# Kernel tuning notes

Hardware: AMD Instinct MI355X
Metric: run time of the kernel (lower is better)

The kernel has to match this reference:

```python
import jax, jax.numpy as jnp
import numpy as np

B, T, D, E, WR, H = 4, 2048, 1024, 4, 128, 4096  # batch, seq, d_model, mem_experts, read width, fuse hidden
EPS = 1e-5


def _ln(u, g, b):
    mu = jnp.mean(u, axis=-1, keepdims=True)
    var = jnp.mean(jnp.square(u - mu), axis=-1, keepdims=True)
    return (u - mu) * jax.lax.rsqrt(var + EPS) * g + b


def setup_inputs() -> dict:
    key = jax.random.key(0)
    ks = jax.random.split(key, 8)
    s1 = 1.0 / np.sqrt(D + WR)
    s2 = 1.0 / np.sqrt(H)
    sg = 1.0 / np.sqrt((1 + E) * D)
    return {
        "x": jax.random.normal(ks[0], (B, T, D), jnp.float32),
        "vt": jax.random.normal(ks[1], (B, T, D), jnp.float32),
        "dts": jax.random.normal(ks[2], (E, B, T, D), jnp.float32),
        "r_feat": jax.random.normal(ks[3], (B, T, WR), jnp.float32),
        "fuse_ln_g": jnp.ones((D + WR,), jnp.float32),
        "fuse_ln_b": jnp.zeros((D + WR,), jnp.float32),
        "fuse_w1": jax.random.normal(ks[4], (D + WR, H), jnp.float32) * s1,
        "fuse_b1": jnp.zeros((H,), jnp.float32),
        "fuse_w2": jax.random.normal(ks[5], (H, D), jnp.float32) * s2,
        "fuse_b2": jnp.zeros((D,), jnp.float32),
        "pg_ln_g": jnp.ones(((1 + E) * D,), jnp.float32),
        "pg_ln_b": jnp.zeros(((1 + E) * D,), jnp.float32),
        "gate_w": jax.random.normal(ks[6], ((1 + E) * D, 1 + E), jnp.float32) * sg,
        "gate_b": jnp.concatenate([jnp.zeros((1,)), jnp.full((E,), -1.0)]).astype(jnp.float32),
    }


def reference(x, vt, dts, r_feat, fuse_ln_g, fuse_ln_b, fuse_w1, fuse_b1,
              fuse_w2, fuse_b2, pg_ln_g, pg_ln_b, gate_w, gate_b):
    # fusion branch: vt = vt + MLP(LN(cat(x, read_feat)))
    fuse_in = jnp.concatenate([x, r_feat], axis=-1)            # [B,T,D+WR]
    h = jax.nn.gelu(_ln(fuse_in, fuse_ln_g, fuse_ln_b) @ fuse_w1 + fuse_b1)
    vt = vt + (h @ fuse_w2 + fuse_b2)

    # paths = [vanilla] + mem experts -> [P,B,T,D], P = 1+E
    paths = jnp.concatenate([vt[None], dts], axis=0)
    z = jnp.moveaxis(paths, 0, -2).reshape(x.shape[0], x.shape[1], -1)  # cat over last dim
    logits = _ln(z, pg_ln_g, pg_ln_b) @ gate_w + gate_b        # temp = 1.0
    pi = jax.nn.softmax(logits, axis=-1)                        # [B,T,P]

    out = jnp.einsum('btp,pbtd->btd', pi, paths)
    g_mem = jnp.sum(pi[..., 1:], axis=-1, keepdims=True)        # synthetic memory gate
    return out, g_mem
```

## Files before the change

kernel.cpp:

```cpp
#include <hip/hip_runtime.h>
#include <hip/hip_bf16.h>

#define Bc 4
#define Tc 2048
#define Dc 1024
#define Ec 4
#define WRc 128
#define Hc 4096
#define Mc (Bc*Tc)
#define K1c (Dc+WRc)
#define Pc (1+Ec)
#define ZDc (Pc*Dc)
#define EPSc 1e-5f

typedef __attribute__((ext_vector_type(8))) short short8;
typedef __attribute__((ext_vector_type(4))) float f32x4;

__device__ __forceinline__ float wave_red_sum(float v) {
    #pragma unroll
    for (int o = 32; o > 0; o >>= 1) v += __shfl_down(v, o);
    return v;
}

__device__ __forceinline__ float gelu_tanh(float x) {
    const float c = 0.7978845608028654f;
    float x3 = x * x * x;
    return 0.5f * x * (1.0f + tanhf(c * (x + 0.044715f * x3)));
}

__global__ __launch_bounds__(256) void transpose_cast_kernel(
    const float* __restrict__ src, __hip_bfloat16* __restrict__ dst, int R, int C) {
    __shared__ float tile[32][33];
    int c0 = blockIdx.x * 32, r0 = blockIdx.y * 32;
    int tx = threadIdx.x, ty = threadIdx.y;
    #pragma unroll
    for (int i = ty; i < 32; i += 8)
        tile[i][tx] = src[(size_t)(r0 + i) * C + c0 + tx];
    __syncthreads();
    #pragma unroll
    for (int i = ty; i < 32; i += 8)
        dst[(size_t)(c0 + i) * R + r0 + tx] = __float2bfloat16(tile[tx][i]);
}

__global__ __launch_bounds__(256) void fuse_ln_kernel(
    const float* __restrict__ x, const float* __restrict__ rf,
    const float* __restrict__ g, const float* __restrict__ b,
    __hip_bfloat16* __restrict__ aln) {
    int row = blockIdx.x;
    int tid = threadIdx.x, lane = tid & 63, wave = tid >> 6;
    const float* xr = x + (size_t)row * Dc;
    const float* rr = rf + (size_t)row * WRc;

    float v[5];
    float s = 0.f, s2 = 0.f;
    #pragma unroll
    for (int i = 0; i < 4; i++) {
        int idx = tid + i * 256;
        float u = xr[idx];
        v[i] = u; s += u; s2 += u * u;
    }
    {
        int idx = tid + 1024;
        float u = (idx < K1c) ? rr[idx - Dc] : 0.f;
        v[4] = u; s += u; s2 += u * u;
    }
    __shared__ float red[8];
    float sw = wave_red_sum(s), s2w = wave_red_sum(s2);
    if (lane == 0) { red[wave] = sw; red[4 + wave] = s2w; }
    __syncthreads();
    float stot  = red[0] + red[1] + red[2] + red[3];
    float s2tot = red[4] + red[5] + red[6] + red[7];
    const float inv = 1.0f / (float)K1c;
    float mu = stot * inv;
    float var = s2tot * inv - mu * mu;
    float rstd = rsqrtf(var + EPSc);

    __hip_bfloat16* orow = aln + (size_t)row * K1c;
    #pragma unroll
    for (int i = 0; i < 4; i++) {
        int idx = tid + i * 256;
        orow[idx] = __float2bfloat16((v[i] - mu) * rstd * g[idx] + b[idx]);
    }
    {
        int idx = tid + 1024;
        if (idx < K1c)
            orow[idx] = __float2bfloat16((v[4] - mu) * rstd * g[idx] + b[idx]);
    }
}

template <int EPI>
__global__ __launch_bounds__(256) void gemm128_kernel(
    const __hip_bfloat16* __restrict__ A, const __hip_bfloat16* __restrict__ Bt,
    int K, int N, const float* __restrict__ bias, const float* __restrict__ add,
    void* __restrict__ outp) {
    __shared__ __hip_bfloat16 As[128 * 64];
    __shared__ __hip_bfloat16 Bs[128 * 64];
    const int tid  = threadIdx.x;
    const int lane = tid & 63;
    const int wave = tid >> 6;
    const int wr = wave >> 1, wc = wave & 1;
    const int m0 = blockIdx.y * 128;
    const int n0 = blockIdx.x * 128;

    f32x4 acc[4][4] = {};

    for (int k0 = 0; k0 < K; k0 += 64) {
        __syncthreads();
        #pragma unroll
        for (int i = 0; i < 4; i++) {
            int f = i * 256 + tid;
            int r = f >> 3, c8 = (f & 7) << 3;
            __builtin_amdgcn_global_load_lds(
                (const __attribute__((address_space(1))) void*)(A + (size_t)(m0 + r) * K + k0 + c8),
                (__attribute__((address_space(3))) void*)(As + f * 8), 16, 0, 0);
        }
        #pragma unroll
        for (int i = 0; i < 4; i++) {
            int f = i * 256 + tid;
            int r = f >> 3, c8 = (f & 7) << 3;
            __builtin_amdgcn_global_load_lds(
                (const __attribute__((address_space(1))) void*)(Bt + (size_t)(n0 + r) * K + k0 + c8),
                (__attribute__((address_space(3))) void*)(Bs + f * 8), 16, 0, 0);
        }
        __syncthreads();

        #pragma unroll
        for (int kk = 0; kk < 2; kk++) {
            short8 af[4], bfr[4];
            #pragma unroll
            for (int m = 0; m < 4; m++)
                af[m] = *(const short8*)(As + (wr * 64 + m * 16 + (lane & 15)) * 64 + kk * 32 + (lane >> 4) * 8);
            #pragma unroll
            for (int n = 0; n < 4; n++)
                bfr[n] = *(const short8*)(Bs + (wc * 64 + n * 16 + (lane & 15)) * 64 + kk * 32 + (lane >> 4) * 8);
            #pragma unroll
            for (int m = 0; m < 4; m++)
                #pragma unroll
                for (int n = 0; n < 4; n++)
                    acc[m][n] = __builtin_amdgcn_mfma_f32_16x16x32_bf16(af[m], bfr[n], acc[m][n], 0, 0, 0);
        }
    }

    #pragma unroll
    for (int m = 0; m < 4; m++) {
        int grow_base = m0 + wr * 64 + m * 16 + (lane >> 4) * 4;
        #pragma unroll
        for (int n = 0; n < 4; n++) {
            int gcol = n0 + wc * 64 + n * 16 + (lane & 15);
            float bv = bias[gcol];
            #pragma unroll
            for (int i = 0; i < 4; i++) {
                int grow = grow_base + i;
                float vv = acc[m][n][i] + bv;
                if (EPI == 0) {
                    ((__hip_bfloat16*)outp)[(size_t)grow * N + gcol] = __float2bfloat16(gelu_tanh(vv));
                } else {
                    ((float*)outp)[(size_t)grow * N + gcol] = vv + add[(size_t)grow * N + gcol];
                }
            }
        }
    }
}

__global__ __launch_bounds__(256) void gate_kernel(
    const float* __restrict__ vtn, const float* __restrict__ dts,
    const float* __restrict__ g, const float* __restrict__ b,
    const float* __restrict__ gw, const float* __restrict__ gb,
    float* __restrict__ out, float* __restrict__ gmem) {
    int row = blockIdx.x;
    int tid = threadIdx.x, lane = tid & 63, wave = tid >> 6;
    __shared__ float z[ZDc];
    __shared__ float red[8];
    __shared__ float lsum[5];
    if (tid < 5) lsum[tid] = 0.f;

    float s = 0.f, s2 = 0.f;
    #pragma unroll
    for (int k = 0; k < ZDc / 256; k++) {
        int i = tid + k * 256;
        int p = i >> 10, d = i & 1023;
        float u = (p == 0) ? vtn[(size_t)row * Dc + d]
                           : dts[((size_t)(p - 1) * Mc + row) * Dc + d];
        z[i] = u; s += u; s2 += u * u;
    }
    float sw = wave_red_sum(s), s2w = wave_red_sum(s2);
    if (lane == 0) { red[wave] = sw; red[4 + wave] = s2w; }
    __syncthreads();
    float stot  = red[0] + red[1] + red[2] + red[3];
    float s2tot = red[4] + red[5] + red[6] + red[7];
    const float inv = 1.0f / (float)ZDc;
    float mu = stot * inv;
    float var = s2tot * inv - mu * mu;
    float rstd = rsqrtf(var + EPSc);

    float lacc[5] = {0.f, 0.f, 0.f, 0.f, 0.f};
    #pragma unroll
    for (int k = 0; k < ZDc / 256; k++) {
        int i = tid + k * 256;
        float zh = (z[i] - mu) * rstd * g[i] + b[i];
        #pragma unroll
        for (int j = 0; j < 5; j++) lacc[j] += zh * gw[i * 5 + j];
    }
    #pragma unroll
    for (int j = 0; j < 5; j++) {
        float v = wave_red_sum(lacc[j]);
        if (lane == 0) atomicAdd(&lsum[j], v);
    }
    __syncthreads();

    float lg[5];
    #pragma unroll
    for (int j = 0; j < 5; j++) lg[j] = lsum[j] + gb[j];
    float mx = lg[0];
    #pragma unroll
    for (int j = 1; j < 5; j++) mx = fmaxf(mx, lg[j]);
    float ex[5], den = 0.f;
    #pragma unroll
    for (int j = 0; j < 5; j++) { ex[j] = expf(lg[j] - mx); den += ex[j]; }
    float rden = 1.0f / den;
    float pi[5];
    #pragma unroll
    for (int j = 0; j < 5; j++) pi[j] = ex[j] * rden;

    #pragma unroll
    for (int k = 0; k < Dc / 256; k++) {
        int d = tid + k * 256;
        float o = 0.f;
        #pragma unroll
        for (int p = 0; p < 5; p++) o += pi[p] * z[p * Dc + d];
        out[(size_t)row * Dc + d] = o;
    }
    if (tid == 0) gmem[row] = pi[1] + pi[2] + pi[3] + pi[4];
}

extern "C" void kernel_launch(void* const* d_in, const int* in_sizes, int n_in,
                              void* d_out, int out_size, void* d_ws, size_t ws_size,
                              hipStream_t stream) {
    const float* x    = (const float*)d_in[0];
    const float* vt   = (const float*)d_in[1];
    const float* dts  = (const float*)d_in[2];
    const float* rf   = (const float*)d_in[3];
    const float* flg  = (const float*)d_in[4];
    const float* flb  = (const float*)d_in[5];
    const float* w1   = (const float*)d_in[6];
    const float* b1   = (const float*)d_in[7];
    const float* w2   = (const float*)d_in[8];
    const float* b2   = (const float*)d_in[9];
    const float* plg  = (const float*)d_in[10];
    const float* plb  = (const float*)d_in[11];
    const float* gw   = (const float*)d_in[12];
    const float* gb   = (const float*)d_in[13];

    char* ws = (char*)d_ws;
    size_t off = 0;
    __hip_bfloat16* w1t = (__hip_bfloat16*)(ws + off); off += (size_t)Hc * K1c * 2;
    __hip_bfloat16* w2t = (__hip_bfloat16*)(ws + off); off += (size_t)Dc * Hc * 2;
    __hip_bfloat16* aln = (__hip_bfloat16*)(ws + off); off += (size_t)Mc * K1c * 2;
    __hip_bfloat16* h   = (__hip_bfloat16*)(ws + off); off += (size_t)Mc * Hc * 2;
    float*          vtn = (float*)(ws + off);          off += (size_t)Mc * Dc * 4;

    transpose_cast_kernel<<<dim3(Hc / 32, K1c / 32), dim3(32, 8), 0, stream>>>(w1, w1t, K1c, Hc);
    transpose_cast_kernel<<<dim3(Dc / 32, Hc / 32), dim3(32, 8), 0, stream>>>(w2, w2t, Hc, Dc);

    fuse_ln_kernel<<<Mc, 256, 0, stream>>>(x, rf, flg, flb, aln);

    gemm128_kernel<0><<<dim3(Hc / 128, Mc / 128), 256, 0, stream>>>(aln, w1t, K1c, Hc, b1, nullptr, h);

    gemm128_kernel<1><<<dim3(Dc / 128, Mc / 128), 256, 0, stream>>>(h, w2t, Hc, Dc, b2, vt, vtn);

    float* outp = (float*)d_out;
    gate_kernel<<<Mc, 256, 0, stream>>>(vtn, dts, plg, plb, gw, gb, outp, outp + (size_t)Mc * Dc);
}
```

Measured before the change: 584.6 us.

## Template GEMM with block swizzle, narrower N tile, and vectorized LN/gate kernels

The GEMM becomes a compile-time-shaped template with a 1D grid whose block index is swizzled across groups of eight, which is meant to spread neighbouring tiles across XCDs and improve L2 reuse. The second GEMM uses a 64-wide N tile so more blocks are launched for the narrow K=4096 output. The layernorm and gate kernels switch to float4 loads and stores. The gate weights are transposed into a workspace buffer so each thread can read them with coalesced vector loads. The smaller N tile lowers arithmetic intensity per block, and an extra small kernel is added to the launch sequence.

Measured after the change: 602.0 us. 3.0% more time.

```diff
diff --git a/kernel.cpp b/kernel.cpp
--- a/kernel.cpp
+++ b/kernel.cpp
@@ -14,6 +14,7 @@
 #define EPSc 1e-5f
 
 typedef __attribute__((ext_vector_type(8))) short short8;
+typedef __attribute__((ext_vector_type(4))) short short4v;
 typedef __attribute__((ext_vector_type(4))) float f32x4;
 
 __device__ __forceinline__ float wave_red_sum(float v) {
@@ -26,6 +27,13 @@
     const float c = 0.7978845608028654f;
     float x3 = x * x * x;
     return 0.5f * x * (1.0f + tanhf(c * (x + 0.044715f * x3)));
+}
+
+__device__ __forceinline__ void store_bf16x4(__hip_bfloat16* p, f32x4 v) {
+    __hip_bfloat16 t[4];
+    t[0] = __float2bfloat16(v[0]); t[1] = __float2bfloat16(v[1]);
+    t[2] = __float2bfloat16(v[2]); t[3] = __float2bfloat16(v[3]);
+    *(short4v*)p = *(const short4v*)t;
 }
 
 __global__ __launch_bounds__(256) void transpose_cast_kernel(
@@ -40,6 +48,13 @@
     #pragma unroll
     for (int i = ty; i < 32; i += 8)
         dst[(size_t)(c0 + i) * R + r0 + tx] = __float2bfloat16(tile[tx][i]);
+}
+
+__global__ __launch_bounds__(256) void gwT_kernel(
+    const float* __restrict__ gw, float* __restrict__ gwT) {
+    int i = blockIdx.x * 256 + threadIdx.x;
+    #pragma unroll
+    for (int j = 0; j < Pc; j++) gwT[j * ZDc + i] = gw[i * Pc + j];
 }
 
 __global__ __launch_bounds__(256) void fuse_ln_kernel(
@@ -48,22 +63,17 @@
     __hip_bfloat16* __restrict__ aln) {
     int row = blockIdx.x;
     int tid = threadIdx.x, lane = tid & 63, wave = tid >> 6;
-    const float* xr = x + (size_t)row * Dc;
-    const float* rr = rf + (size_t)row * WRc;
-
-    float v[5];
-    float s = 0.f, s2 = 0.f;
-    #pragma unroll
-    for (int i = 0; i < 4; i++) {
-        int idx = tid + i * 256;
-        float u = xr[idx];
-        v[i] = u; s += u; s2 += u * u;
-    }
-    {
-        int idx = tid + 1024;
-        float u = (idx < K1c) ? rr[idx - Dc] : 0.f;
-        v[4] = u; s += u; s2 += u * u;
-    }
+    const f32x4* x4 = (const f32x4*)(x + (size_t)row * Dc);
+    const f32x4* r4 = (const f32x4*)(rf + (size_t)row * WRc);
+
+    f32x4 v0 = x4[tid];
+    f32x4 v1 = {0.f, 0.f, 0.f, 0.f};
+    if (tid < 32) v1 = r4[tid];
+
+    float s  = v0[0]+v0[1]+v0[2]+v0[3] + v1[0]+v1[1]+v1[2]+v1[3];
+    float s2 = v0[0]*v0[0]+v0[1]*v0[1]+v0[2]*v0[2]+v0[3]*v0[3]
+             + v1[0]*v1[0]+v1[1]*v1[1]+v1[2]*v1[2]+v1[3]*v1[3];
+
     __shared__ float red[8];
     float sw = wave_red_sum(s), s2w = wave_red_sum(s2);
     if (lane == 0) { red[wave] = sw; red[4 + wave] = s2w; }
@@ -76,86 +86,98 @@
     float rstd = rsqrtf(var + EPSc);
 
     __hip_bfloat16* orow = aln + (size_t)row * K1c;
-    #pragma unroll
-    for (int i = 0; i < 4; i++) {
-        int idx = tid + i * 256;
-        orow[idx] = __float2bfloat16((v[i] - mu) * rstd * g[idx] + b[idx]);
-    }
     {
-        int idx = tid + 1024;
-        if (idx < K1c)
-            orow[idx] = __float2bfloat16((v[4] - mu) * rstd * g[idx] + b[idx]);
-    }
-}
-
-template <int EPI>
-__global__ __launch_bounds__(256) void gemm128_kernel(
+        f32x4 gg = *(const f32x4*)(g + tid * 4);
+        f32x4 bb = *(const f32x4*)(b + tid * 4);
+        f32x4 o  = (v0 - mu) * rstd * gg + bb;
+        store_bf16x4(orow + tid * 4, o);
+    }
+    if (tid < 32) {
+        f32x4 gg = *(const f32x4*)(g + 1024 + tid * 4);
+        f32x4 bb = *(const f32x4*)(b + 1024 + tid * 4);
+        f32x4 o  = (v1 - mu) * rstd * gg + bb;
+        store_bf16x4(orow + 1024 + tid * 4, o);
+    }
+}
+
+template <int Mdim, int Ndim, int Kdim, int BN, int EPI>
+__global__ __launch_bounds__(256) void gemm_kernel(
     const __hip_bfloat16* __restrict__ A, const __hip_bfloat16* __restrict__ Bt,
-    int K, int N, const float* __restrict__ bias, const float* __restrict__ add,
+    const float* __restrict__ bias, const float* __restrict__ add,
     void* __restrict__ outp) {
-    __shared__ __hip_bfloat16 As[128 * 64];
-    __shared__ __hip_bfloat16 Bs[128 * 64];
+    constexpr int BM = 128, BK = 64;
+    constexpr int WN = BN / 2;
+    constexpr int MF = 4, NF = WN / 16;
+    constexpr int NTN = Ndim / BN;
+    constexpr int NT  = (Mdim / BM) * NTN;
+    constexpr int GB  = BN * 8 / 256;
+
+    __shared__ __hip_bfloat16 As[BM * BK];
+    __shared__ __hip_bfloat16 Bs[BN * BK];
+
     const int tid  = threadIdx.x;
     const int lane = tid & 63;
     const int wave = tid >> 6;
     const int wr = wave >> 1, wc = wave & 1;
-    const int m0 = blockIdx.y * 128;
-    const int n0 = blockIdx.x * 128;
-
-    f32x4 acc[4][4] = {};
-
-    for (int k0 = 0; k0 < K; k0 += 64) {
+
+    constexpr int CPX = NT / 8;
+    int bid = blockIdx.x;
+    int swz = (bid & 7) * CPX + (bid >> 3);
+    const int m0 = (swz / NTN) * BM;
+    const int n0 = (swz % NTN) * BN;
+
+    const __hip_bfloat16* ag = A  + (size_t)(m0 + (tid >> 3)) * Kdim + (tid & 7) * 8;
+    const __hip_bfloat16* bg = Bt + (size_t)(n0 + (tid >> 3)) * Kdim + (tid & 7) * 8;
+
+    f32x4 acc[MF][NF] = {};
+
+    for (int k0 = 0; k0 < Kdim; k0 += BK) {
         __syncthreads();
         #pragma unroll
-        for (int i = 0; i < 4; i++) {
-            int f = i * 256 + tid;
-            int r = f >> 3, c8 = (f & 7) << 3;
+        for (int i = 0; i < 4; i++)
             __builtin_amdgcn_global_load_lds(
-                (const __attribute__((address_space(1))) void*)(A + (size_t)(m0 + r) * K + k0 + c8),
-                (__attribute__((address_space(3))) void*)(As + f * 8), 16, 0, 0);
+                (const __attribute__((address_space(1))) void*)(ag + (size_t)i * 32 * Kdim),
+                (__attribute__((address_space(3))) void*)(As + (i * 256 + tid) * 8), 16, 0, 0);
+        #pragma unroll
+        for (int i = 0; i < GB; i++)
+            __builtin_amdgcn_global_load_lds(
+                (const __attribute__((address_space(1))) void*)(bg + (size_t)i * 32 * Kdim),
+                (__attribute__((address_space(3))) void*)(Bs + (i * 256 + tid) * 8), 16, 0, 0);
+        ag += BK; bg += BK;
+        __syncthreads();
+
+        #pragma unroll
+        for (int kk = 0; kk < 2; kk++) {
+            short8 af[MF], bf[NF];
+            #pragma unroll
+            for (int m = 0; m < MF; m++)
+                af[m] = *(const short8*)(As + (wr * 64 + m * 16 + (lane & 15)) * BK + kk * 32 + (lane >> 4) * 8);
+            #pragma unroll
+            for (int n = 0; n < NF; n++)
+                bf[n] = *(const short8*)(Bs + (wc * WN + n * 16 + (lane & 15)) * BK + kk * 32 + (lane >> 4) * 8);
+            #pragma unroll
+            for (int m = 0; m < MF; m++)
+                #pragma unroll
+                for (int n = 0; n < NF; n++)
+                    acc[m][n] = __builtin_amdgcn_mfma_f32_16x16x32_bf16(af[m], bf[n], acc[m][n], 0, 0, 0);
         }
-        #pragma unroll
-        for (int i = 0; i < 4; i++) {
-            int f = i * 256 + tid;
-            int r = f >> 3, c8 = (f & 7) << 3;
-            __builtin_amdgcn_global_load_lds(
-                (const __attribute__((address_space(1))) void*)(Bt + (size_t)(n0 + r) * K + k0 + c8),
-                (__attribute__((address_space(3))) void*)(Bs + f * 8), 16, 0, 0);
-        }
-        __syncthreads();
-
-        #pragma unroll
-        for (int kk = 0; kk < 2; kk++) {
-            short8 af[4], bfr[4];
-            #pragma unroll
-            for (int m = 0; m < 4; m++)
-                af[m] = *(const short8*)(As + (wr * 64 + m * 16 + (lane & 15)) * 64 + kk * 32 + (lane >> 4) * 8);
-            #pragma unroll
-            for (int n = 0; n < 4; n++)
-                bfr[n] = *(const short8*)(Bs + (wc * 64 + n * 16 + (lane & 15)) * 64 + kk * 32 + (lane >> 4) * 8);
-            #pragma unroll
-            for (int m = 0; m < 4; m++)
-                #pragma unroll
-                for (int n = 0; n < 4; n++)
-                    acc[m][n] = __builtin_amdgcn_mfma_f32_16x16x32_bf16(af[m], bfr[n], acc[m][n], 0, 0, 0);
-        }
-    }
-
-    #pragma unroll
-    for (int m = 0; m < 4; m++) {
+    }
+
+    #pragma unroll
+    for (int m = 0; m < MF; m++) {
         int grow_base = m0 + wr * 64 + m * 16 + (lane >> 4) * 4;
         #pragma unroll
-        for (int n = 0; n < 4; n++) {
-            int gcol = n0 + wc * 64 + n * 16 + (lane & 15);
+        for (int n = 0; n < NF; n++) {
+            int gcol = n0 + wc * WN + n * 16 + (lane & 15);
             float bv = bias[gcol];
             #pragma unroll
             for (int i = 0; i < 4; i++) {
                 int grow = grow_base + i;
                 float vv = acc[m][n][i] + bv;
                 if (EPI == 0) {
-                    ((__hip_bfloat16*)outp)[(size_t)grow * N + gcol] = __float2bfloat16(gelu_tanh(vv));
+                    ((__hip_bfloat16*)outp)[(size_t)grow * Ndim + gcol] = __float2bfloat16(gelu_tanh(vv));
                 } else {
-                    ((float*)outp)[(size_t)grow * N + gcol] = vv + add[(size_t)grow * N + gcol];
+                    ((float*)outp)[(size_t)grow * Ndim + gcol] = vv + add[(size_t)grow * Ndim + gcol];
                 }
             }
         }
@@ -165,23 +187,27 @@
 __global__ __launch_bounds__(256) void gate_kernel(
     const float* __restrict__ vtn, const float* __restrict__ dts,
     const float* __restrict__ g, const float* __restrict__ b,
-    const float* __restrict__ gw, const float* __restrict__ gb,
+    const float* __restrict__ gwT, const float* __restrict__ gb,
     float* __restrict__ out, float* __restrict__ gmem) {
     int row = blockIdx.x;
     int tid = threadIdx.x, lane = tid & 63, wave = tid >> 6;
-    __shared__ float z[ZDc];
+    __shared__ f32x4 z4[ZDc / 4];
     __shared__ float red[8];
-    __shared__ float lsum[5];
-    if (tid < 5) lsum[tid] = 0.f;
-
+    __shared__ float lsum[Pc];
+    if (tid < Pc) lsum[tid] = 0.f;
+
+    const f32x4* vt4 = (const f32x4*)(vtn + (size_t)row * Dc);
     float s = 0.f, s2 = 0.f;
     #pragma unroll
-    for (int k = 0; k < ZDc / 256; k++) {
-        int i = tid + k * 256;
-        int p = i >> 10, d = i & 1023;
-        float u = (p == 0) ? vtn[(size_t)row * Dc + d]
-                           : dts[((size_t)(p - 1) * Mc + row) * Dc + d];
-        z[i] = u; s += u; s2 += u * u;
+    for (int k = 0; k < 5; k++) {
+        int i4 = tid + k * 256;
+        int p  = i4 >> 8;
+        int d4 = i4 & 255;
+        f32x4 u = (p == 0) ? vt4[d4]
+                : *(const f32x4*)(dts + ((size_t)(p - 1) * Mc + row) * Dc + d4 * 4);
+        z4[i4] = u;
+        s  += u[0] + u[1] + u[2] + u[3];
+        s2 += u[0]*u[0] + u[1]*u[1] + u[2]*u[2] + u[3]*u[3];
     }
     float sw = wave_red_sum(s), s2w = wave_red_sum(s2);
     if (lane == 0) { red[wave] = sw; red[4 + wave] = s2w; }
@@ -193,43 +219,45 @@
     float var = s2tot * inv - mu * mu;
     float rstd = rsqrtf(var + EPSc);
 
-    float lacc[5] = {0.f, 0.f, 0.f, 0.f, 0.f};
-    #pragma unroll
-    for (int k = 0; k < ZDc / 256; k++) {
-        int i = tid + k * 256;
-        float zh = (z[i] - mu) * rstd * g[i] + b[i];
-        #pragma unroll
-        for (int j = 0; j < 5; j++) lacc[j] += zh * gw[i * 5 + j];
-    }
-    #pragma unroll
-    for (int j = 0; j < 5; j++) {
+    float lacc[Pc] = {0.f, 0.f, 0.f, 0.f, 0.f};
+    #pragma unroll
+    for (int k = 0; k < 5; k++) {
+        int i4 = tid + k * 256;
+        f32x4 zz = z4[i4];
+        f32x4 gg = *(const f32x4*)(g + i4 * 4);
+        f32x4 bb = *(const f32x4*)(b + i4 * 4);
+        f32x4 zh = (zz - mu) * rstd * gg + bb;
+        #pragma unroll
+        for (int j = 0; j < Pc; j++) {
+            f32x4 w = *(const f32x4*)(gwT + j * ZDc + i4 * 4);
+            lacc[j] += zh[0]*w[0] + zh[1]*w[1] + zh[2]*w[2] + zh[3]*w[3];
+        }
+    }
+    #pragma unroll
+    for (int j = 0; j < Pc; j++) {
         float v = wave_red_sum(lacc[j]);
         if (lane == 0) atomicAdd(&lsum[j], v);
     }
     __syncthreads();
 
-    float lg[5];
-    #pragma unroll
-    for (int j = 0; j < 5; j++) lg[j] = lsum[j] + gb[j];
+    float lg[Pc];
+    #pragma unroll
+    for (int j = 0; j < Pc; j++) lg[j] = lsum[j] + gb[j];
     float mx = lg[0];
     #pragma unroll
-    for (int j = 1; j < 5; j++) mx = fmaxf(mx, lg[j]);
-    float ex[5], den = 0.f;
-    #pragma unroll
-    for (int j = 0; j < 5; j++) { ex[j] = expf(lg[j] - mx); den += ex[j]; }
+    for (int j = 1; j < Pc; j++) mx = fmaxf(mx, lg[j]);
+    float ex[Pc], den = 0.f;
+    #pragma unroll
+    for (int j = 0; j < Pc; j++) { ex[j] = expf(lg[j] - mx); den += ex[j]; }
     float rden = 1.0f / den;
-    float pi[5];
-    #pragma unroll
-    for (int j = 0; j < 5; j++) pi[j] = ex[j] * rden;
-
-    #pragma unroll
-    for (int k = 0; k < Dc / 256; k++) {
-        int d = tid + k * 256;
-        float o = 0.f;
-        #pragma unroll
-        for (int p = 0; p < 5; p++) o += pi[p] * z[p * Dc + d];
-        out[(size_t)row * Dc + d] = o;
-    }
+    float pi[Pc];
+    #pragma unroll
+    for (int j = 0; j < Pc; j++) pi[j] = ex[j] * rden;
+
+    f32x4 o = {0.f, 0.f, 0.f, 0.f};
+    #pragma unroll
+    for (int p = 0; p < Pc; p++) o += pi[p] * z4[p * 256 + tid];
+    *(f32x4*)(out + (size_t)row * Dc + tid * 4) = o;
     if (tid == 0) gmem[row] = pi[1] + pi[2] + pi[3] + pi[4];
 }
 
@@ -258,16 +286,20 @@
     __hip_bfloat16* aln = (__hip_bfloat16*)(ws + off); off += (size_t)Mc * K1c * 2;
     __hip_bfloat16* h   = (__hip_bfloat16*)(ws + off); off += (size_t)Mc * Hc * 2;
     float*          vtn = (float*)(ws + off);          off += (size_t)Mc * Dc * 4;
+    float*          gwT = (float*)(ws + off);          off += (size_t)Pc * ZDc * 4;
 
     transpose_cast_kernel<<<dim3(Hc / 32, K1c / 32), dim3(32, 8), 0, stream>>>(w1, w1t, K1c, Hc);
     transpose_cast_kernel<<<dim3(Dc / 32, Hc / 32), dim3(32, 8), 0, stream>>>(w2, w2t, Hc, Dc);
+    gwT_kernel<<<ZDc / 256, 256, 0, stream>>>(gw, gwT);
 
     fuse_ln_kernel<<<Mc, 256, 0, stream>>>(x, rf, flg, flb, aln);
 
-    gemm128_kernel<0><<<dim3(Hc / 128, Mc / 128), 256, 0, stream>>>(aln, w1t, K1c, Hc, b1, nullptr, h);
-
-    gemm128_kernel<1><<<dim3(Dc / 128, Mc / 128), 256, 0, stream>>>(h, w2t, Hc, Dc, b2, vt, vtn);
+    gemm_kernel<Mc, Hc, K1c, 128, 0><<<(Mc / 128) * (Hc / 128), 256, 0, stream>>>(
+        aln, w1t, b1, nullptr, h);
+
+    gemm_kernel<Mc, Dc, Hc, 64, 1><<<(Mc / 128) * (Dc / 64), 256, 0, stream>>>(
+        h, w2t, b2, vt, vtn);
 
     float* outp = (float*)d_out;
-    gate_kernel<<<Mc, 256, 0, stream>>>(vtn, dts, plg, plb, gw, gb, outp, outp + (size_t)Mc * Dc);
-}
+    gate_kernel<<<Mc, 256, 0, stream>>>(vtn, dts, plg, plb, gwT, gb, outp, outp + (size_t)Mc * Dc);
+}
```
